# Optimization experiments

Measured on AMD Instinct MI355X. Metric: run time of the kernel, lower is better.

Reference implementation:

```python
import jax, jax.numpy as jnp
import numpy as np

D_MODEL = 1024
D_FF = 4096
N_HEADS = 16
D_HEAD = D_MODEL // N_HEADS
BSZ, SEQ = 2, 2048
EPS = 1e-6


def layer_norm(x, lam, beta):
    # torch impl: (x - mu) / (std_biased + eps) * lambda + beta
    mu = jnp.mean(x, axis=-1, keepdims=True)
    sigma = jnp.sqrt(jnp.mean((x - mu) ** 2, axis=-1, keepdims=True)) + EPS
    return (x - mu) / sigma * lam + beta


def setup_inputs() -> dict:
    key = jax.random.key(0)
    ks = jax.random.split(key, 10)
    s = 0.02
    x = jax.random.normal(ks[0], (BSZ, SEQ, D_MODEL), dtype=jnp.float32)
    mask = jnp.ones((BSZ, 1, 1, SEQ), dtype=jnp.int32)
    # nn.Linear weights stored [out, in]; y = x @ W.T
    Wq = jax.random.normal(ks[1], (D_MODEL, D_MODEL), dtype=jnp.float32) * s
    Wk = jax.random.normal(ks[2], (D_MODEL, D_MODEL), dtype=jnp.float32) * s
    Wv = jax.random.normal(ks[3], (D_MODEL, D_MODEL), dtype=jnp.float32) * s
    Wo = jax.random.normal(ks[4], (D_MODEL, D_MODEL), dtype=jnp.float32) * s
    w1 = jax.random.normal(ks[5], (D_FF, D_MODEL), dtype=jnp.float32) * s
    b1 = jnp.zeros((D_FF,), dtype=jnp.float32)
    w2 = jax.random.normal(ks[6], (D_MODEL, D_FF), dtype=jnp.float32) * s
    b2 = jnp.zeros((D_MODEL,), dtype=jnp.float32)
    g1 = jnp.ones((D_MODEL,), dtype=jnp.float32)
    be1 = jnp.zeros((D_MODEL,), dtype=jnp.float32)
    g2 = jnp.ones((D_MODEL,), dtype=jnp.float32)
    be2 = jnp.zeros((D_MODEL,), dtype=jnp.float32)
    return {"x": x, "mask": mask, "Wq": Wq, "Wk": Wk, "Wv": Wv, "Wo": Wo,
            "w1": w1, "b1": b1, "w2": w2, "b2": b2,
            "g1": g1, "be1": be1, "g2": g2, "be2": be2}


def reference(x, mask, Wq, Wk, Wv, Wo, w1, b1, w2, b2, g1, be1, g2, be2):
    b, s, _ = x.shape
    # projections (y = x @ W.T), split heads -> [b, h, s, dh]
    def split_heads(t):
        return t.reshape(b, s, N_HEADS, D_HEAD).transpose(0, 2, 1, 3)
    Q = split_heads(x @ Wq.T)
    K = split_heads(x @ Wk.T)
    V = split_heads(x @ Wv.T)
    score = jnp.einsum('bhqd,bhkd->bhqk', Q, K) / jnp.sqrt(jnp.float32(D_HEAD))
    score = jnp.where(mask == 0, -jnp.inf, score)
    attn = jax.nn.softmax(score, axis=-1)
    out = jnp.einsum('bhqk,bhkd->bhqd', attn, V)
    out = out.transpose(0, 2, 1, 3).reshape(b, s, D_MODEL)
    x1 = out @ Wo.T
    x2 = layer_norm(x1 + x, g1, be1)
    x3 = jax.nn.relu(x2 @ w1.T + b1) @ w2.T + b2
    x4 = layer_norm(x2 + x3, g2, be2)
    return x4
```

## Files before the change

### kernel.cpp

```cpp
#include <hip/hip_runtime.h>
#include <math.h>

typedef __attribute__((ext_vector_type(8))) short bf16x8;
typedef __attribute__((ext_vector_type(4))) float f32x4;
typedef __attribute__((ext_vector_type(8))) unsigned short us8;
typedef unsigned short u16;
typedef unsigned int u32;

constexpr int BSZ = 2, SEQ = 2048, DM = 1024, DFF = 4096, NH = 16, DH = 64;
constexpr int MROWS = BSZ * SEQ;

__device__ __forceinline__ float bf2f(u16 u) {
  union { unsigned int i; float f; } v; v.i = ((unsigned int)u) << 16; return v.f;
}
__device__ __forceinline__ u16 f2bf(float f) {
  union { float f; unsigned int i; } v; v.f = f;
  unsigned int r = v.i + 0x7fffu + ((v.i >> 16) & 1u);
  return (u16)(r >> 16);
}

#define GLOAD16(gp, lp) __builtin_amdgcn_global_load_lds( \
    (const __attribute__((address_space(1))) void*)(gp),  \
    (__attribute__((address_space(3))) void*)(lp), 16, 0, 0)
#define GLOAD4(gp, lp) __builtin_amdgcn_global_load_lds( \
    (const __attribute__((address_space(1))) void*)(gp),  \
    (__attribute__((address_space(3))) void*)(lp), 4, 0, 0)

__global__ __launch_bounds__(256) void cvt_all(
    const float* __restrict__ x, const float* __restrict__ Wq,
    const float* __restrict__ Wk, const float* __restrict__ Wv,
    const float* __restrict__ Wo, const float* __restrict__ w1,
    const float* __restrict__ w2, u16* __restrict__ xb,
    u16* __restrict__ Wqkvb, u16* __restrict__ Wob,
    u16* __restrict__ w1b, u16* __restrict__ w2b) {
  constexpr int M1 = 1 << 20;
  const int i = (blockIdx.x * 256 + threadIdx.x) * 8;
  const float* src;
  u16* dst;
  int off;
  if (i < 4 * M1)        { src = x;  dst = xb;            off = i;           }
  else if (i < 5 * M1)   { src = Wq; dst = Wqkvb;         off = i - 4 * M1;  }
  else if (i < 6 * M1)   { src = Wk; dst = Wqkvb + M1;    off = i - 5 * M1;  }
  else if (i < 7 * M1)   { src = Wv; dst = Wqkvb + 2 * M1; off = i - 6 * M1; }
  else if (i < 8 * M1)   { src = Wo; dst = Wob;           off = i - 7 * M1;  }
  else if (i < 12 * M1)  { src = w1; dst = w1b;           off = i - 8 * M1;  }
  else                   { src = w2; dst = w2b;           off = i - 12 * M1; }
  const float4 a = *(const float4*)(src + off);
  const float4 b = *(const float4*)(src + off + 4);
  uint4 o;
  o.x = f2bf(a.x) | ((unsigned)f2bf(a.y) << 16);
  o.y = f2bf(a.z) | ((unsigned)f2bf(a.w) << 16);
  o.z = f2bf(b.x) | ((unsigned)f2bf(b.y) << 16);
  o.w = f2bf(b.z) | ((unsigned)f2bf(b.w) << 16);
  *(uint4*)(dst + off) = o;
}

template <int BM, int BN, bool BIAS, bool RELU>
__global__ __launch_bounds__(256) void gemm_bf16(
    const u16* __restrict__ A, const u16* __restrict__ B,
    const float* __restrict__ bias, u16* __restrict__ Cb,
    int M, int N, int K, int ld) {
  constexpr int MI = BM / 32, NI = BN / 32;
  __shared__ u16 As[2][BM * 32];
  __shared__ u16 Bs[2][BN * 32];
  const int tid = threadIdx.x;
  const int lane = tid & 63, wid = tid >> 6;

  const int nwg = gridDim.x * gridDim.y;
  int id = blockIdx.y * gridDim.x + blockIdx.x;
  id = (id & 7) * (nwg >> 3) + (id >> 3);
  const int bx = id % gridDim.x, by = id / gridDim.x;

  const u16* Az = A + (size_t)blockIdx.z * K;
  const u16* Bz = B + (size_t)blockIdx.z * K;
  u16* Cz = Cb + (size_t)blockIdx.z * M * N;

  const int row0 = by * BM, col0 = bx * BN;
  const int wr = (wid >> 1) * (BM / 2), wc = (wid & 1) * (BN / 2);
  const int fr = lane & 15, hi = lane >> 4;

  f32x4 acc[MI][NI];
#pragma unroll
  for (int i = 0; i < MI; ++i)
#pragma unroll
    for (int j = 0; j < NI; ++j) acc[i][j] = {0.f, 0.f, 0.f, 0.f};

  const int sr = tid >> 2;
  const int se = (tid & 3) * 8;

#define STAGE(buf, k0)                                                        \
  {                                                                           \
    _Pragma("unroll")                                                         \
    for (int c = 0; c < BM * 64; c += 4096) {                                 \
      const int r = (c >> 6) + sr;                                            \
      GLOAD16(Az + (size_t)(row0 + r) * ld + ((k0) + se),                     \
              ((char*)As[buf]) + c + tid * 16);                               \
    }                                                                         \
    _Pragma("unroll")                                                         \
    for (int c = 0; c < BN * 64; c += 4096) {                                 \
      const int r = (c >> 6) + sr;                                            \
      GLOAD16(Bz + (size_t)(col0 + r) * ld + ((k0) + se),                     \
              ((char*)Bs[buf]) + c + tid * 16);                               \
    }                                                                         \
  }

  STAGE(0, 0);
  __syncthreads();

  const int NIT = K / 32;
  for (int it = 0; it < NIT; ++it) {
    const int cur = it & 1;
    if (it + 1 < NIT) STAGE(cur ^ 1, (it + 1) * 32);

    bf16x8 af[MI], bv[NI];
#pragma unroll
    for (int mi = 0; mi < MI; ++mi)
      af[mi] = *(const bf16x8*)&As[cur][(wr + mi * 16 + fr) * 32 + hi * 8];
#pragma unroll
    for (int ni = 0; ni < NI; ++ni)
      bv[ni] = *(const bf16x8*)&Bs[cur][(wc + ni * 16 + fr) * 32 + hi * 8];
#pragma unroll
    for (int mi = 0; mi < MI; ++mi)
#pragma unroll
      for (int ni = 0; ni < NI; ++ni)
        acc[mi][ni] = __builtin_amdgcn_mfma_f32_16x16x32_bf16(
            af[mi], bv[ni], acc[mi][ni], 0, 0, 0);
    __syncthreads();
  }
#undef STAGE

  const int erow = row0 + wr + (hi << 2);
  const int ecol0 = col0 + wc;
#pragma unroll
  for (int ni = 0; ni < NI; ++ni) {
    const int col = ecol0 + ni * 16 + fr;
    const float bvv = BIAS ? bias[col] : 0.f;
#pragma unroll
    for (int mi = 0; mi < MI; ++mi) {
      const int rbase = erow + mi * 16;
#pragma unroll
      for (int j = 0; j < 4; ++j) {
        float v = acc[mi][ni][j] + bvv;
        if (RELU) v = fmaxf(v, 0.f);
        Cz[(size_t)(rbase + j) * N + col] = f2bf(v);
      }
    }
  }
}

__global__ __launch_bounds__(512) void attn_mfma(
    const u16* __restrict__ QKV, const int* __restrict__ mask,
    u16* __restrict__ Ob) {
  constexpr int KB = 64, QB = 128, NT = SEQ / KB;
  __shared__ u16 Kl[2][KB * 64];
  __shared__ u16 Vt[2][64 * KB];
  __shared__ int ml[2][KB];

  const int tid = threadIdx.x;
  const int lane = tid & 63, wid = tid >> 6;
  const int q0 = blockIdx.x * QB;
  const int bh = blockIdx.y;
  const int b = bh >> 4, h = bh & 15;
  const size_t base = (size_t)b * SEQ * 3072;
  const int fr = lane & 15, g = lane >> 4;

  const u16* qp = QKV + base + (size_t)(q0 + wid * 16 + fr) * 3072 + h * 64 + g * 8;
  bf16x8 qf0, qf1;
  {
    const float QSC = 0.18033688f;
    const us8 ua = *(const us8*)qp;
    const us8 ub = *(const us8*)(qp + 32);
    u32 pa[4], pb[4];
#pragma unroll
    for (int i = 0; i < 4; ++i) {
      const float a0 = bf2f(ua[2 * i]) * QSC, a1 = bf2f(ua[2 * i + 1]) * QSC;
      const float b0 = bf2f(ub[2 * i]) * QSC, b1 = bf2f(ub[2 * i + 1]) * QSC;
      asm("v_cvt_pk_bf16_f32 %0, %1, %2" : "=v"(pa[i]) : "v"(a0), "v"(a1));
      asm("v_cvt_pk_bf16_f32 %0, %1, %2" : "=v"(pb[i]) : "v"(b0), "v"(b1));
    }
    union { u32 d[4]; bf16x8 v; } c0, c1;
#pragma unroll
    for (int i = 0; i < 4; ++i) { c0.d[i] = pa[i]; c1.d[i] = pb[i]; }
    qf0 = c0.v; qf1 = c1.v;
  }

  const int krow = wid * 8 + (lane >> 3);
  const int kcol = 8 * ((lane & 7) ^ (lane >> 3));
  const u16* ksrc = QKV + base + 1024 + h * 64 + kcol;
  const int kdst = wid * 1024 + lane * 16;

  const int va = (tid & 255) >> 3;
  const int vq = tid & 7;
  const u16* vsrc = QKV + base + 2048 + h * 64 + vq * 8;
  const bool vstage = (wid < 4);

  f32x4 o[4] = {{0.f,0.f,0.f,0.f},{0.f,0.f,0.f,0.f},{0.f,0.f,0.f,0.f},{0.f,0.f,0.f,0.f}};
  float mreg = -3e38f, lreg = 0.f;

  {
    GLOAD16(ksrc + (size_t)krow * 3072, (char*)Kl[0] + kdst);
    if (wid == 4) GLOAD4(mask + b * SEQ + lane, (char*)ml[0] + lane * 4);
    if (vstage) {
      const us8 v0 = *(const us8*)(vsrc + (size_t)(2 * va) * 3072);
      const us8 v1 = *(const us8*)(vsrc + (size_t)(2 * va + 1) * 3072);
      char* vb = (char*)Vt[0];
#pragma unroll
      for (int i = 0; i < 8; ++i) {
        const int d = vq * 8 + i;
        const u32 wv = (u32)(u16)v0[i] | ((u32)(u16)v1[i] << 16);
        *(u32*)(vb + d * 128 + ((4 * va) ^ ((vq ^ i) << 4))) = wv;
      }
    }
  }
  __syncthreads();

  for (int it = 0; it < NT; ++it) {
    const int cur = it & 1, nxt = cur ^ 1;
    const int ktn = (it + 1) * KB;
    const bool pre = (it + 1 < NT);
    us8 v0 = {}, v1 = {};
    if (pre) {
      GLOAD16(ksrc + (size_t)(ktn + krow) * 3072, (char*)Kl[nxt] + kdst);
      if (wid == 4) GLOAD4(mask + b * SEQ + ktn + lane, (char*)ml[nxt] + lane * 4);
      if (vstage) {
        v0 = *(const us8*)(vsrc + (size_t)(ktn + 2 * va) * 3072);
        v1 = *(const us8*)(vsrc + (size_t)(ktn + 2 * va + 1) * 3072);
      }
    }

    f32x4 s[4];
#pragma unroll
    for (int t16 = 0; t16 < 4; ++t16) {
      const int kr = t16 * 16 + fr;
      const char* krp = (const char*)Kl[cur] + kr * 128;
      const int sw = (kr & 7) << 4;
      const bf16x8 kf0 = *(const bf16x8*)(krp + ((g * 16) ^ sw));
      const bf16x8 kf1 = *(const bf16x8*)(krp + ((g * 16 + 64) ^ sw));
      f32x4 a = {0.f, 0.f, 0.f, 0.f};
      a = __builtin_amdgcn_mfma_f32_16x16x32_bf16(kf0, qf0, a, 0, 0, 0);
      a = __builtin_amdgcn_mfma_f32_16x16x32_bf16(kf1, qf1, a, 0, 0, 0);
      s[t16] = a;
    }

#pragma unroll
    for (int t16 = 0; t16 < 4; ++t16) {
      const int4 mv = *(const int4*)&ml[cur][t16 * 16 + g * 4];
      const int* mp = (const int*)&mv;
#pragma unroll
      for (int j = 0; j < 4; ++j)
        if (mp[j] == 0) s[t16][j] = -3e38f;
    }

    float rmax = s[0][0];
#pragma unroll
    for (int t16 = 0; t16 < 4; ++t16)
#pragma unroll
      for (int j = 0; j < 4; ++j) rmax = fmaxf(rmax, s[t16][j]);

    if (!__all(rmax <= mreg + 12.f)) {
      rmax = fmaxf(rmax, __shfl_xor(rmax, 16));
      rmax = fmaxf(rmax, __shfl_xor(rmax, 32));
      const float mn = fmaxf(mreg, rmax);
      float sc;
      asm("v_exp_f32 %0, %1" : "=v"(sc) : "v"(mreg - mn));
      mreg = mn;
      lreg *= sc;
#pragma unroll
      for (int j = 0; j < 4; ++j) {
        const float scj = __shfl(sc, (g << 4) + g * 4 + j);
#pragma unroll
        for (int dt = 0; dt < 4; ++dt) o[dt][j] *= scj;
      }
    }

    float p[4][4];
#pragma unroll
    for (int t16 = 0; t16 < 4; ++t16)
#pragma unroll
      for (int j = 0; j < 4; ++j) {
        float e;
        asm("v_exp_f32 %0, %1" : "=v"(e) : "v"(s[t16][j] - mreg));
        p[t16][j] = e;
        lreg += e;
      }

    u32 plo[4], phi[4];
#pragma unroll
    for (int t16 = 0; t16 < 4; ++t16) {
      asm("v_cvt_pk_bf16_f32 %0, %1, %2"
          : "=v"(plo[t16]) : "v"(p[t16][0]), "v"(p[t16][1]));
      asm("v_cvt_pk_bf16_f32 %0, %1, %2"
          : "=v"(phi[t16]) : "v"(p[t16][2]), "v"(p[t16][3]));
    }

#pragma unroll
    for (int kh = 0; kh < 2; ++kh) {
      u32 fd[4];
#pragma unroll
      for (int hf = 0; hf < 2; ++hf) {
        const int sl = fr + ((((g & 1) << 1) + hf) << 4);
        const u32 c0l = (u32)__shfl((int)plo[kh * 2], sl);
        const u32 c0h = (u32)__shfl((int)phi[kh * 2], sl);
        const u32 c1l = (u32)__shfl((int)plo[kh * 2 + 1], sl);
        const u32 c1h = (u32)__shfl((int)phi[kh * 2 + 1], sl);
        const bool s1 = ((g >> 1) & 1) != 0;
        fd[hf * 2] = s1 ? c1l : c0l;
        fd[hf * 2 + 1] = s1 ? c1h : c0h;
      }
      union { u32 d[4]; bf16x8 v; } uu;
      uu.d[0] = fd[0]; uu.d[1] = fd[1]; uu.d[2] = fd[2]; uu.d[3] = fd[3];
      const bf16x8 pf = uu.v;
#pragma unroll
      for (int dt = 0; dt < 4; ++dt) {
        const int d = dt * 16 + fr;
        const int xd = (((d >> 3) ^ d) & 7) << 4;
        const bf16x8 vf = *(const bf16x8*)((const char*)Vt[cur] + d * 128 +
                                           ((g * 16 + kh * 64) ^ xd));
        o[dt] = __builtin_amdgcn_mfma_f32_16x16x32_bf16(pf, vf, o[dt], 0, 0, 0);
      }
    }

    if (pre && vstage) {
      char* vb = (char*)Vt[nxt];
#pragma unroll
      for (int i = 0; i < 8; ++i) {
        const int d = vq * 8 + i;
        const u32 wv = (u32)(u16)v0[i] | ((u32)(u16)v1[i] << 16);
        *(u32*)(vb + d * 128 + ((4 * va) ^ ((vq ^ i) << 4))) = wv;
      }
    }
    __syncthreads();
  }

  lreg += __shfl_xor(lreg, 16);
  lreg += __shfl_xor(lreg, 32);
  const float inv = 1.f / lreg;
#pragma unroll
  for (int j = 0; j < 4; ++j) {
    const float invj = __shfl(inv, (g << 4) + g * 4 + j);
    const int qrow = q0 + wid * 16 + g * 4 + j;
    u16* orow = Ob + (size_t)(b * SEQ + qrow) * DM + h * 64;
#pragma unroll
    for (int dt = 0; dt < 4; ++dt)
      orow[dt * 16 + fr] = f2bf(o[dt][j] * invj);
  }
}

template <bool OBF, bool HASC, bool HASB>
__global__ __launch_bounds__(256) void ln_add(
    const u16* __restrict__ Ap, const u16* __restrict__ Bp,
    const u16* __restrict__ Cp, const float* __restrict__ bias,
    const float* __restrict__ g, const float* __restrict__ be,
    void* __restrict__ outp) {
  __shared__ float red[2][4];
  __shared__ float mu_s, sig_s;
  const int row = blockIdx.x;
  const int tid = threadIdx.x;
  const size_t off = (size_t)row * DM + tid * 4;

  const ushort4 ua = *(const ushort4*)(Ap + off);
  const ushort4 ub = *(const ushort4*)(Bp + off);
  float4 s = make_float4(bf2f(ua.x) + bf2f(ub.x), bf2f(ua.y) + bf2f(ub.y),
                         bf2f(ua.z) + bf2f(ub.z), bf2f(ua.w) + bf2f(ub.w));
  if (HASC) {
    const ushort4 uc = *(const ushort4*)(Cp + off);
    s.x += bf2f(uc.x); s.y += bf2f(uc.y); s.z += bf2f(uc.z); s.w += bf2f(uc.w);
  }
  if (HASB) {
    const float4 bb = *(const float4*)(bias + tid * 4);
    s.x += bb.x; s.y += bb.y; s.z += bb.z; s.w += bb.w;
  }

  float sum = s.x + s.y + s.z + s.w;
  float sq = s.x * s.x + s.y * s.y + s.z * s.z + s.w * s.w;
#pragma unroll
  for (int off2 = 32; off2 >= 1; off2 >>= 1) {
    sum += __shfl_xor(sum, off2);
    sq += __shfl_xor(sq, off2);
  }
  const int wid = tid >> 6;
  if ((tid & 63) == 0) { red[0][wid] = sum; red[1][wid] = sq; }
  __syncthreads();
  if (tid == 0) {
    float ts = red[0][0] + red[0][1] + red[0][2] + red[0][3];
    float tq = red[1][0] + red[1][1] + red[1][2] + red[1][3];
    float mu = ts * (1.f / DM);
    float var = tq * (1.f / DM) - mu * mu;
    mu_s = mu;
    sig_s = sqrtf(fmaxf(var, 0.f)) + 1e-6f;
  }
  __syncthreads();
  const float mu = mu_s, inv = 1.f / sig_s;
  const float4 gv = *(const float4*)(g + tid * 4);
  const float4 bv = *(const float4*)(be + tid * 4);
  float4 o;
  o.x = (s.x - mu) * inv * gv.x + bv.x;
  o.y = (s.y - mu) * inv * gv.y + bv.y;
  o.z = (s.z - mu) * inv * gv.z + bv.z;
  o.w = (s.w - mu) * inv * gv.w + bv.w;
  if (OBF) {
    u16* op = (u16*)outp + off;
    ushort4 o4;
    o4.x = f2bf(o.x); o4.y = f2bf(o.y); o4.z = f2bf(o.z); o4.w = f2bf(o.w);
    *(ushort4*)op = o4;
  } else {
    *(float4*)((float*)outp + off) = o;
  }
}

extern "C" void kernel_launch(void* const* d_in, const int* in_sizes, int n_in,
                              void* d_out, int out_size, void* d_ws,
                              size_t ws_size, hipStream_t stream) {
  const float* x  = (const float*)d_in[0];
  const int* mask = (const int*)d_in[1];
  const float* Wq = (const float*)d_in[2];
  const float* Wk = (const float*)d_in[3];
  const float* Wv = (const float*)d_in[4];
  const float* Wo = (const float*)d_in[5];
  const float* w1 = (const float*)d_in[6];
  const float* b1 = (const float*)d_in[7];
  const float* w2 = (const float*)d_in[8];
  const float* b2 = (const float*)d_in[9];
  const float* g1 = (const float*)d_in[10];
  const float* be1 = (const float*)d_in[11];
  const float* g2 = (const float*)d_in[12];
  const float* be2 = (const float*)d_in[13];
  float* out = (float*)d_out;
  float* ws = (float*)d_ws;

  u16*   QKVb  = (u16*)(ws + 0);
  u16*   xb    = (u16*)(ws + 6291456);
  u16*   Wqkvb = (u16*)(ws + 8388608);
  u16*   Wob   = (u16*)(ws + 9961472);
  u16*   w1b   = (u16*)(ws + 10485760);
  u16*   w2b   = (u16*)(ws + 12582912);
  u16*   Obf   = (u16*)(ws + 14680064);
  u16*   X1a   = (u16*)(ws + 16777216);
  u16*   X1c   = (u16*)(ws + 18874368);
  u16*   X2b   = (u16*)(ws + 20971520);
  u16*   X3a   = (u16*)(ws + 23068672);
  u16*   X3c   = (u16*)(ws + 25165824);
  u16*   Hb    = (u16*)(ws + 0);

  const dim3 blk(256);

  cvt_all<<<8192, blk, 0, stream>>>(x, Wq, Wk, Wv, Wo, w1, w2,
                                    xb, Wqkvb, Wob, w1b, w2b);

  gemm_bf16<128, 128, false, false><<<dim3(3072 / 128, MROWS / 128), blk, 0, stream>>>(
      xb, Wqkvb, nullptr, QKVb, MROWS, 3072, DM, DM);

  attn_mfma<<<dim3(SEQ / 128, BSZ * NH), dim3(512), 0, stream>>>(QKVb, mask, Obf);

  gemm_bf16<64, 128, false, false><<<dim3(DM / 128, MROWS / 64, 2), blk, 0, stream>>>(
      Obf, Wob, nullptr, X1a, MROWS, DM, DM / 2, DM);

  ln_add<true, true, false><<<dim3(MROWS), blk, 0, stream>>>(
      X1a, xb, X1c, nullptr, g1, be1, X2b);

  gemm_bf16<128, 128, true, true><<<dim3(DFF / 128, MROWS / 128), blk, 0, stream>>>(
      X2b, w1b, b1, Hb, MROWS, DFF, DM, DM);

  gemm_bf16<64, 128, false, false><<<dim3(DM / 128, MROWS / 64, 2), blk, 0, stream>>>(
      Hb, w2b, nullptr, X3a, MROWS, DM, DFF / 2, DFF);

  ln_add<false, true, true><<<dim3(MROWS), blk, 0, stream>>>(
      X2b, X3a, X3c, b2, g2, be2, out);
}
```

Measured before the change: 262.4 us.

## Split attention over key dimension into two halves with combine kernel

Attention now runs a split-K (flash-decoding style) scheme: each block handles half the key sequence and writes unnormalized bf16 partial outputs plus running max and sum to a workspace. A new combine kernel merges the two partials using exp-weighted rescaling and writes the normalized output. This doubles the attention grid from 512 to 1024 blocks to improve occupancy across CUs, at the cost of an extra kernel launch, extra global traffic for partials, and bf16 rounding of unnormalized partials. The partial buffer overlaps the X1a workspace region, which is only written later.

```diff
diff --git a/kernel.cpp b/kernel.cpp
--- a/kernel.cpp
+++ b/kernel.cpp
@@ -9,6 +9,7 @@
 
 constexpr int BSZ = 2, SEQ = 2048, DM = 1024, DFF = 4096, NH = 16, DH = 64;
 constexpr int MROWS = BSZ * SEQ;
+constexpr int NREC = BSZ * NH * SEQ;
 
 __device__ __forceinline__ float bf2f(u16 u) {
   union { unsigned int i; float f; } v; v.i = ((unsigned int)u) << 16; return v.f;
@@ -150,8 +151,8 @@
 
 __global__ __launch_bounds__(512) void attn_mfma(
     const u16* __restrict__ QKV, const int* __restrict__ mask,
-    u16* __restrict__ Ob) {
-  constexpr int KB = 64, QB = 128, NT = SEQ / KB;
+    char* __restrict__ Pp) {
+  constexpr int KB = 64, QB = 128, NTS = SEQ / KB / 2;
   __shared__ u16 Kl[2][KB * 64];
   __shared__ u16 Vt[2][64 * KB];
   __shared__ int ml[2][KB];
@@ -160,6 +161,8 @@
   const int lane = tid & 63, wid = tid >> 6;
   const int q0 = blockIdx.x * QB;
   const int bh = blockIdx.y;
+  const int z = blockIdx.z;
+  const int kt0 = z * (SEQ / 2);
   const int b = bh >> 4, h = bh & 15;
   const size_t base = (size_t)b * SEQ * 3072;
   const int fr = lane & 15, g = lane >> 4;
@@ -198,11 +201,11 @@
   float mreg = -3e38f, lreg = 0.f;
 
   {
-    GLOAD16(ksrc + (size_t)krow * 3072, (char*)Kl[0] + kdst);
-    if (wid == 4) GLOAD4(mask + b * SEQ + lane, (char*)ml[0] + lane * 4);
+    GLOAD16(ksrc + (size_t)(kt0 + krow) * 3072, (char*)Kl[0] + kdst);
+    if (wid == 4) GLOAD4(mask + b * SEQ + kt0 + lane, (char*)ml[0] + lane * 4);
     if (vstage) {
-      const us8 v0 = *(const us8*)(vsrc + (size_t)(2 * va) * 3072);
-      const us8 v1 = *(const us8*)(vsrc + (size_t)(2 * va + 1) * 3072);
+      const us8 v0 = *(const us8*)(vsrc + (size_t)(kt0 + 2 * va) * 3072);
+      const us8 v1 = *(const us8*)(vsrc + (size_t)(kt0 + 2 * va + 1) * 3072);
       char* vb = (char*)Vt[0];
 #pragma unroll
       for (int i = 0; i < 8; ++i) {
@@ -214,10 +217,10 @@
   }
   __syncthreads();
 
-  for (int it = 0; it < NT; ++it) {
+  for (int it = 0; it < NTS; ++it) {
     const int cur = it & 1, nxt = cur ^ 1;
-    const int ktn = (it + 1) * KB;
-    const bool pre = (it + 1 < NT);
+    const int ktn = kt0 + (it + 1) * KB;
+    const bool pre = (it + 1 < NTS);
     us8 v0 = {}, v1 = {};
     if (pre) {
       GLOAD16(ksrc + (size_t)(ktn + krow) * 3072, (char*)Kl[nxt] + kdst);
@@ -334,16 +337,45 @@
 
   lreg += __shfl_xor(lreg, 16);
   lreg += __shfl_xor(lreg, 32);
-  const float inv = 1.f / lreg;
 #pragma unroll
   for (int j = 0; j < 4; ++j) {
-    const float invj = __shfl(inv, (g << 4) + g * 4 + j);
+    const int sl = (g << 4) + g * 4 + j;
+    const float lj = __shfl(lreg, sl);
+    const float mj = __shfl(mreg, sl);
     const int qrow = q0 + wid * 16 + g * 4 + j;
-    u16* orow = Ob + (size_t)(b * SEQ + qrow) * DM + h * 64;
+    const int r = bh * SEQ + qrow;
+    char* rec = Pp + ((size_t)z * NREC + r) * 136;
+    u16* rn = (u16*)rec;
 #pragma unroll
     for (int dt = 0; dt < 4; ++dt)
-      orow[dt * 16 + fr] = f2bf(o[dt][j] * invj);
-  }
+      rn[dt * 16 + fr] = f2bf(o[dt][j]);
+    if (fr == 0) {
+      ((float*)rec)[32] = mj;
+      ((float*)rec)[33] = lj;
+    }
+  }
+}
+
+__global__ __launch_bounds__(256) void attn_combine(
+    const char* __restrict__ Pp, u16* __restrict__ Ob) {
+  const int tid = threadIdx.x;
+  const int w = tid >> 6, d = tid & 63;
+  const int r = blockIdx.x * 4 + w;
+  const char* r0 = Pp + (size_t)r * 136;
+  const char* r1 = r0 + (size_t)NREC * 136;
+  const float m0 = *(const float*)(r0 + 128), l0 = *(const float*)(r0 + 132);
+  const float m1 = *(const float*)(r1 + 128), l1 = *(const float*)(r1 + 132);
+  const float M = fmaxf(m0, m1);
+  float w0, w1;
+  asm("v_exp_f32 %0, %1" : "=v"(w0) : "v"(m0 - M));
+  asm("v_exp_f32 %0, %1" : "=v"(w1) : "v"(m1 - M));
+  const float n0 = bf2f(((const u16*)r0)[d]);
+  const float n1 = bf2f(((const u16*)r1)[d]);
+  const float num = w0 * n0 + w1 * n1;
+  const float den = w0 * l0 + w1 * l1;
+  const int bh = r >> 11, q = r & 2047;
+  const int b = bh >> 4, h = bh & 15;
+  Ob[((size_t)(b * SEQ + q)) * DM + h * 64 + d] = f2bf(num / den);
 }
 
 template <bool OBF, bool HASC, bool HASB>
@@ -435,6 +467,7 @@
   u16*   w1b   = (u16*)(ws + 10485760);
   u16*   w2b   = (u16*)(ws + 12582912);
   u16*   Obf   = (u16*)(ws + 14680064);
+  char*  Pp    = (char*)(ws + 16777216);
   u16*   X1a   = (u16*)(ws + 16777216);
   u16*   X1c   = (u16*)(ws + 18874368);
   u16*   X2b   = (u16*)(ws + 20971520);
@@ -450,7 +483,8 @@
   gemm_bf16<128, 128, false, false><<<dim3(3072 / 128, MROWS / 128), blk, 0, stream>>>(
       xb, Wqkvb, nullptr, QKVb, MROWS, 3072, DM, DM);
 
-  attn_mfma<<<dim3(SEQ / 128, BSZ * NH), dim3(512), 0, stream>>>(QKVb, mask, Obf);
+  attn_mfma<<<dim3(SEQ / 128, BSZ * NH, 2), dim3(512), 0, stream>>>(QKVb, mask, Pp);
+  attn_combine<<<dim3(NREC / 4), blk, 0, stream>>>(Pp, Obf);
 
   gemm_bf16<64, 128, false, false><<<dim3(DM / 128, MROWS / 64, 2), blk, 0, stream>>>(
       Obf, Wob, nullptr, X1a, MROWS, DM, DM / 2, DM);
```

After: 272.2 us. 1.04x slower.
